# Optimization experiments

Measured on AMD Instinct MI355X. Metric: run time of the kernel, lower is better.

## Reference

```python
import jax, jax.numpy as jnp
import numpy as np

BETA = 0.25  # commitment loss weight (init kwarg)


def setup_inputs() -> dict:
    key = jax.random.key(0)
    k1, k2 = jax.random.split(key)
    z = jax.random.normal(k1, (16, 256, 32, 32), dtype=jnp.float32)
    embedding = jax.random.normal(k2, (8192, 256), dtype=jnp.float32)
    return {"z": z, "embedding": embedding}


def reference(z, embedding):
    # z: [B, C, H, W]  embedding: [K, C]
    B, C, H, W = z.shape
    zp = jnp.transpose(z, (0, 2, 3, 1))            # [B, H, W, C]
    zf = zp.reshape(-1, C)                          # [N, C]
    # squared euclidean distances via ||z||^2 + ||e||^2 - 2 z.e : [N, K]
    d = (jnp.sum(zf * zf, axis=1, keepdims=True)
         + jnp.sum(embedding * embedding, axis=1)
         - 2.0 * jnp.einsum('nd,kd->nk', zf, embedding))
    min_encoding_indices = jnp.argmin(d, axis=1)    # [N]
    z_q = embedding[min_encoding_indices].reshape(zp.shape)  # [B, H, W, C]
    loss = (BETA * jnp.mean((jax.lax.stop_gradient(z_q) - zp) ** 2)
            + jnp.mean((z_q - jax.lax.stop_gradient(zp)) ** 2))
    # straight-through estimator
    z_q = zp + jax.lax.stop_gradient(z_q - zp)
    z_q = jnp.transpose(z_q, (0, 3, 1, 2))          # back to [B, C, H, W]
    return z_q, loss, min_encoding_indices
```

## Files before the change

### kernel.cpp

```cpp
#include <hip/hip_runtime.h>

typedef unsigned int u32;
typedef unsigned long long u64;

#define C_DIM 256
#define HW 1024
#define N_TOT 16384
#define K_DIM 8192
#define ZQ_SIZE 4194304
#define LOSS_OFF ZQ_SIZE
#define IDX_OFF (ZQ_SIZE + 1)

#define KRANGE 2048
#define MARGIN 2.0f
#define CAP 524288u
#define LCAP 8192u

#define WS_ENORM 0
#define WS_CNT 8192
#define WS_PACKED 16384
#define WS_FIDX 49152
#define WS_LPART 65536
#define WS_LIST 131072
#define WS_ZT32 1179648
#define WS_ZTB16 5373952
#define WS_EB16 7471104

typedef __attribute__((ext_vector_type(4))) float f32x4;
typedef __attribute__((ext_vector_type(8))) __bf16 bf16x8;
typedef __attribute__((ext_vector_type(8))) unsigned short u16x8;

__device__ __forceinline__ void gld_lds16(const void* g, void* l) {
    __builtin_amdgcn_global_load_lds(
        (const __attribute__((address_space(1))) u32*)g,
        (__attribute__((address_space(3))) u32*)l, 16, 0, 0);
}

__device__ __forceinline__ unsigned short f2bf(float f) {
    u32 u = __float_as_uint(f);
    u32 r = (u + 0x7FFFu + ((u >> 16) & 1u)) >> 16;
    return (unsigned short)r;
}

__global__ __launch_bounds__(256) void k_prep_e(const float* __restrict__ e,
                                                unsigned short* __restrict__ eb,
                                                float* __restrict__ enorm1) {
    int w = threadIdx.x >> 6, l = threadIdx.x & 63;
    int row = blockIdx.x * 4 + w;
    const float4 v = *reinterpret_cast<const float4*>(e + (size_t)row * C_DIM + l * 4);
    float s = v.x * v.x + v.y * v.y + v.z * v.z + v.w * v.w;
    #pragma unroll
    for (int off = 32; off; off >>= 1) s += __shfl_xor(s, off, 64);
    if (l == 0) enorm1[row] = s + 1024.0f;
    ushort4 h;
    h.x = f2bf(v.x); h.y = f2bf(v.y); h.z = f2bf(v.z); h.w = f2bf(v.w);
    *reinterpret_cast<ushort4*>(eb + (size_t)row * C_DIM + l * 4) = h;
}

__global__ __launch_bounds__(256) void k_prep_z(const float* __restrict__ z,
                                                float* __restrict__ zt32,
                                                unsigned short* __restrict__ ztb) {
    int bid = blockIdx.x;
    int b = bid >> 7;
    int hwt = (bid >> 3) & 15;
    int ct = bid & 7;
    int t = threadIdx.x;
    __shared__ float tile[32][65];
    #pragma unroll
    for (int p = 0; p < 8; ++p) {
        int cl = p * 4 + (t >> 6), hl = t & 63;
        tile[cl][hl] = z[((size_t)b << 18) + ((size_t)(ct * 32 + cl) << 10) + hwt * 64 + hl];
    }
    __syncthreads();
    int hl = t & 63, cg = t >> 6;
    int n = (b << 10) + hwt * 64 + hl;
    float v[8];
    #pragma unroll
    for (int j = 0; j < 8; ++j) v[j] = tile[cg * 8 + j][hl];
    size_t base = (size_t)n * C_DIM + ct * 32 + cg * 8;
    *reinterpret_cast<float4*>(zt32 + base) = make_float4(v[0], v[1], v[2], v[3]);
    *reinterpret_cast<float4*>(zt32 + base + 4) = make_float4(v[4], v[5], v[6], v[7]);
    u16x8 h;
    #pragma unroll
    for (int j = 0; j < 8; ++j) h[j] = f2bf(v[j]);
    *reinterpret_cast<u16x8*>(ztb + base) = h;
}

__global__ __launch_bounds__(256, 2) void k_screen(const unsigned short* __restrict__ zt,
                                                   const unsigned short* __restrict__ et,
                                                   const float* __restrict__ enorm1,
                                                   u32* __restrict__ cnt,
                                                   uint2* __restrict__ list) {
    __shared__ __align__(16) char lds[81920];
    char* Ab = lds;
    char* Bb = lds + 65536;

    int logical = (blockIdx.x & 7) * 64 + (blockIdx.x >> 3);
    const int ks = logical >> 7;
    const int rowtile = logical & 127;
    const int n0 = rowtile * 128;
    const int kbase = ks * KRANGE;

    const int tid = threadIdx.x;
    const int l = tid & 63, w = tid >> 6;
    const int wr = w >> 1, wc = w & 1;
    const int ll = l & 15, lh = l >> 4;

    #pragma unroll
    for (int j = 0; j < 16; ++j) {
        int Y = (w * 16 + j) * 1024 + l * 16;
        int row = Y >> 9;
        int slot = (Y >> 4) & 31;
        const char* src = (const char*)zt + (((size_t)(n0 + row)) << 9) + ((slot ^ (row & 7)) << 4);
        gld_lds16(src, Ab + (w * 16 + j) * 1024);
    }

    const char* srcB[2];
    char* dstB[2];
    #pragma unroll
    for (int j = 0; j < 2; ++j) {
        int D = w * 128 + j * 64 + l;
        int rB = D >> 2;
        int sB = (D & 3) ^ ((rB >> 1) & 3);
        srcB[j] = (const char*)et + ((size_t)(kbase + rB) << 9) + (sB << 4);
        dstB[j] = Bb + (w * 128 + j * 64) * 16;
    }

    int aoff[4], rxA[4];
    #pragma unroll
    for (int mf = 0; mf < 4; ++mf) {
        int row = wr * 64 + mf * 16 + ll;
        aoff[mf] = row * 512;
        rxA[mf] = row & 7;
    }
    int bfrOff[4];
    #pragma unroll
    for (int kf = 0; kf < 4; ++kf) {
        int row = wc * 64 + kf * 16 + ll;
        bfrOff[kf] = (row * 4 + (lh ^ ((row >> 1) & 3))) * 16;
    }

    f32x4 acc[4][4];
    #pragma unroll
    for (int a = 0; a < 4; ++a)
        #pragma unroll
        for (int b = 0; b < 4; ++b) acc[a][b] = (f32x4){0.f, 0.f, 0.f, 0.f};
    float m1[16], m2[16];
    #pragma unroll
    for (int s = 0; s < 16; ++s) { m1[s] = 3.4e38f; m2[s] = 3.4e38f; }

    gld_lds16(srcB[0], dstB[0]);
    gld_lds16(srcB[1], dstB[1]);
    __syncthreads();

    for (int it = 0; it < 16; ++it) {
        float en[4];
        #pragma unroll
        for (int kf = 0; kf < 4; ++kf)
            en[kf] = enorm1[kbase + it * 128 + wc * 64 + kf * 16 + ll];

        #pragma unroll
        for (int cs = 0; cs < 8; ++cs) {
            const int p = cs & 1;
            if (it < 15 || cs < 7) {
                const size_t koff = (size_t)it * 65536 + ((cs == 7) ? 65536 : (cs + 1) * 64);
                gld_lds16(srcB[0] + koff, dstB[0] + (p ^ 1) * 8192);
                gld_lds16(srcB[1] + koff, dstB[1] + (p ^ 1) * 8192);
            }
            bf16x8 af[4], bfr[4];
            #pragma unroll
            for (int mf = 0; mf < 4; ++mf)
                af[mf] = *reinterpret_cast<const bf16x8*>(
                    Ab + aoff[mf] + (((cs * 4 + lh) ^ rxA[mf]) << 4));
            #pragma unroll
            for (int kf = 0; kf < 4; ++kf)
                bfr[kf] = *reinterpret_cast<const bf16x8*>(Bb + p * 8192 + bfrOff[kf]);
            __builtin_amdgcn_s_setprio(1);
            #pragma unroll
            for (int mf = 0; mf < 4; ++mf)
                #pragma unroll
                for (int kf = 0; kf < 4; ++kf)
                    acc[mf][kf] = __builtin_amdgcn_mfma_f32_16x16x32_bf16(
                        af[mf], bfr[kf], acc[mf][kf], 0, 0, 0);
            __builtin_amdgcn_s_setprio(0);

            if (cs == 7) {
                #pragma unroll
                for (int kf = 0; kf < 4; ++kf) {
                    const u32 kcol = (u32)(kbase + it * 128 + wc * 64 + kf * 16 + ll);
                    #pragma unroll
                    for (int mf = 0; mf < 4; ++mf) {
                        #pragma unroll
                        for (int r = 0; r < 4; ++r) {
                            float d = fmaf(-2.0f, acc[mf][kf][r], en[kf]);
                            float df = __uint_as_float((__float_as_uint(d) & 0xFFFFE000u) | kcol);
                            const int s2 = mf * 4 + r;
                            float t = fmaxf(m1[s2], df);
                            m2[s2] = fminf(m2[s2], t);
                            m1[s2] = fminf(m1[s2], df);
                            acc[mf][kf][r] = 0.0f;
                        }
                    }
                }
            }
            __syncthreads();
        }
    }

    float rowm[16];
    #pragma unroll
    for (int s = 0; s < 16; ++s) rowm[s] = m1[s];
    #pragma unroll
    for (int m = 1; m <= 8; m <<= 1)
        #pragma unroll
        for (int s = 0; s < 16; ++s)
            rowm[s] = fminf(rowm[s], __shfl_xor(rowm[s], m, 64));

    float* LDSrm = (float*)Bb;
    float* LDSrmF = (float*)(Bb + 1024);
    u32* ccnt = (u32*)(Bb + 1536);
    u32* gbase = (u32*)(Bb + 1540);
    uint2* cbuf = (uint2*)Ab;

    if (ll == 0) {
        #pragma unroll
        for (int s = 0; s < 16; ++s) {
            int row_local = wr * 64 + (s >> 2) * 16 + lh * 4 + (s & 3);
            LDSrm[row_local * 2 + wc] = rowm[s];
        }
    }
    if (tid == 0) *ccnt = 0;
    __syncthreads();
    if (tid < 128)
        LDSrmF[tid] = fminf(LDSrm[tid * 2], LDSrm[tid * 2 + 1]);
    __syncthreads();

    #pragma unroll
    for (int s = 0; s < 16; ++s) {
        int row_local = wr * 64 + (s >> 2) * 16 + lh * 4 + (s & 3);
        float rm = __uint_as_float(__float_as_uint(LDSrmF[row_local]) & 0xFFFFE000u);
        float d1 = __uint_as_float(__float_as_uint(m1[s]) & 0xFFFFE000u);
        if (d1 <= rm + MARGIN) {
            u32 pos = atomicAdd(ccnt, 1u);
            uint2 ent = make_uint2((u32)(n0 + row_local), __float_as_uint(m1[s]) & 8191u);
            if (pos < LCAP) cbuf[pos] = ent;
            else { u32 gp = atomicAdd(cnt, 1u); if (gp < CAP) list[gp] = ent; }
        }
        float d2 = __uint_as_float(__float_as_uint(m2[s]) & 0xFFFFE000u);
        if (d2 <= rm + MARGIN) {
            for (int it2 = 0; it2 < 16; ++it2) {
                #pragma unroll
                for (int kf = 0; kf < 4; ++kf) {
                    u32 k = (u32)(kbase + it2 * 128 + wc * 64 + kf * 16 + ll);
                    u32 pos = atomicAdd(ccnt, 1u);
                    uint2 ent = make_uint2((u32)(n0 + row_local), k);
                    if (pos < LCAP) cbuf[pos] = ent;
                    else { u32 gp = atomicAdd(cnt, 1u); if (gp < CAP) list[gp] = ent; }
                }
            }
        }
    }
    __syncthreads();
    if (tid == 0) {
        u32 total = *ccnt; if (total > LCAP) total = LCAP;
        *gbase = atomicAdd(cnt, total);
    }
    __syncthreads();
    u32 total = *ccnt; if (total > LCAP) total = LCAP;
    u32 gb = *gbase;
    for (u32 i = tid; i < total; i += 256) {
        u32 gp = gb + i;
        if (gp < CAP) list[gp] = cbuf[i];
    }
}

__global__ __launch_bounds__(256) void k_exact(const float* __restrict__ zt32,
                                               const float* __restrict__ e,
                                               const float* __restrict__ enorm1,
                                               const u32* __restrict__ cnt,
                                               const uint2* __restrict__ list,
                                               u64* __restrict__ packed) {
    const int nw = gridDim.x * 4;
    const int wid = blockIdx.x * 4 + (threadIdx.x >> 6);
    const int l = threadIdx.x & 63;
    u32 total = *cnt;
    if (total > CAP) total = CAP;
    for (u32 i = wid; i < total; i += nw) {
        uint2 c = list[i];
        const float4 zv = *reinterpret_cast<const float4*>(zt32 + (size_t)c.x * C_DIM + l * 4);
        const float4 ev = *reinterpret_cast<const float4*>(e + (size_t)c.y * C_DIM + l * 4);
        float s = zv.x * ev.x + zv.y * ev.y + zv.z * ev.z + zv.w * ev.w;
        #pragma unroll
        for (int off = 32; off; off >>= 1) s += __shfl_xor(s, off, 64);
        if (l == 0) {
            float d = fmaf(-2.0f, s, enorm1[c.y]);
            u32 ub = __float_as_uint(d);
            ub = (ub & 0x80000000u) ? ~ub : (ub | 0x80000000u);
            u64 key = ((u64)ub << 32) | (u64)c.y;
            atomicMin(packed + c.x, key);
        }
    }
}

__global__ __launch_bounds__(256) void k_fin(const u64* __restrict__ packed,
                                             int* __restrict__ fidx,
                                             float* __restrict__ out_idx) {
    int n = blockIdx.x * 256 + threadIdx.x;
    if (n >= N_TOT) return;
    u32 kk = (u32)(packed[n] & 0xFFFFFFFFull);
    if (kk > 8191u) kk = 0u;
    fidx[n] = (int)kk;
    out_idx[n] = (float)kk;
}

#define GBLOCKS 2048
__global__ __launch_bounds__(256) void k_gather(const float* __restrict__ z,
                                                const float* __restrict__ e,
                                                const int* __restrict__ fidx,
                                                float* __restrict__ zq,
                                                float* __restrict__ lpart) {
    float s = 0.0f;
    for (int i = blockIdx.x * 256 + threadIdx.x; i < ZQ_SIZE; i += GBLOCKS * 256) {
        int bb = i >> 18;
        int c = (i >> 10) & 255;
        int hw = i & 1023;
        int n = (bb << 10) | hw;
        float q = e[(size_t)fidx[n] * C_DIM + c];
        float zv = z[i];
        zq[i] = q;
        float d = q - zv;
        s = fmaf(d, d, s);
    }
    #pragma unroll
    for (int off = 32; off; off >>= 1) s += __shfl_xor(s, off, 64);
    __shared__ float wsum[4];
    int lane = threadIdx.x & 63, w = threadIdx.x >> 6;
    if (lane == 0) wsum[w] = s;
    __syncthreads();
    if (threadIdx.x == 0) lpart[blockIdx.x] = wsum[0] + wsum[1] + wsum[2] + wsum[3];
}

__global__ __launch_bounds__(256) void k_loss(const float* __restrict__ lpart,
                                              float* __restrict__ out_loss) {
    float s = 0.0f;
    for (int i = threadIdx.x; i < GBLOCKS; i += 256) s += lpart[i];
    #pragma unroll
    for (int off = 32; off; off >>= 1) s += __shfl_xor(s, off, 64);
    __shared__ float wsum[4];
    int lane = threadIdx.x & 63, w = threadIdx.x >> 6;
    if (lane == 0) wsum[w] = s;
    __syncthreads();
    if (threadIdx.x == 0)
        out_loss[0] = (wsum[0] + wsum[1] + wsum[2] + wsum[3]) * (1.25f / (float)ZQ_SIZE);
}

extern "C" void kernel_launch(void* const* d_in, const int* in_sizes, int n_in,
                              void* d_out, int out_size, void* d_ws, size_t ws_size,
                              hipStream_t stream) {
    const float* z = (const float*)d_in[0];
    const float* e = (const float*)d_in[1];
    float* out = (float*)d_out;
    float* ws = (float*)d_ws;

    float* enorm1 = ws + WS_ENORM;
    u32* cnt = (u32*)(ws + WS_CNT);
    u64* packed = (u64*)(ws + WS_PACKED);
    int* fidx = (int*)(ws + WS_FIDX);
    float* lpart = ws + WS_LPART;
    uint2* list = (uint2*)(ws + WS_LIST);
    float* zt32 = ws + WS_ZT32;
    unsigned short* ztb = (unsigned short*)(ws + WS_ZTB16);
    unsigned short* eb = (unsigned short*)(ws + WS_EB16);

    hipMemsetAsync(cnt, 0, sizeof(u32), stream);
    hipMemsetAsync(packed, 0xFF, (size_t)N_TOT * sizeof(u64), stream);

    k_prep_e<<<dim3(K_DIM / 4), dim3(256), 0, stream>>>(e, eb, enorm1);
    k_prep_z<<<dim3(2048), dim3(256), 0, stream>>>(z, zt32, ztb);
    k_screen<<<dim3(512), dim3(256), 0, stream>>>(ztb, eb, enorm1, cnt, list);
    k_exact<<<dim3(1024), dim3(256), 0, stream>>>(zt32, e, enorm1, cnt, list, packed);
    k_fin<<<dim3(64), dim3(256), 0, stream>>>(packed, fidx, out + IDX_OFF);
    k_gather<<<dim3(GBLOCKS), dim3(256), 0, stream>>>(z, e, fidx, out, lpart);
    k_loss<<<dim3(1), dim3(256), 0, stream>>>(lpart, out + LOSS_OFF);
}
```

Baseline: 194.2 us.

## Load codebook fragments directly into registers in screen kernel; fuse finalize into gather

The screening GEMM no longer stages the bf16 codebook through double-buffered LDS. Each lane now loads its B fragments straight from global memory into registers, ping-ponging between two register sets, which removes the per-step __syncthreads and shrinks LDS use. The separate k_fin kernel is folded into k_gather, which decodes the packed argmin key itself and writes the index output. The trade is more scattered global and L2 traffic for B in place of LDS reuse across waves, plus one fewer launch.

```diff
diff --git a/kernel.cpp b/kernel.cpp
--- a/kernel.cpp
+++ b/kernel.cpp
@@ -19,7 +19,6 @@
 #define WS_ENORM 0
 #define WS_CNT 8192
 #define WS_PACKED 16384
-#define WS_FIDX 49152
 #define WS_LPART 65536
 #define WS_LIST 131072
 #define WS_ZT32 1179648
@@ -91,9 +90,8 @@
                                                    const float* __restrict__ enorm1,
                                                    u32* __restrict__ cnt,
                                                    uint2* __restrict__ list) {
-    __shared__ __align__(16) char lds[81920];
+    __shared__ __align__(16) char lds[67088];
     char* Ab = lds;
-    char* Bb = lds + 65536;
 
     int logical = (blockIdx.x & 7) * 64 + (blockIdx.x >> 3);
     const int ks = logical >> 7;
@@ -115,17 +113,6 @@
         gld_lds16(src, Ab + (w * 16 + j) * 1024);
     }
 
-    const char* srcB[2];
-    char* dstB[2];
-    #pragma unroll
-    for (int j = 0; j < 2; ++j) {
-        int D = w * 128 + j * 64 + l;
-        int rB = D >> 2;
-        int sB = (D & 3) ^ ((rB >> 1) & 3);
-        srcB[j] = (const char*)et + ((size_t)(kbase + rB) << 9) + (sB << 4);
-        dstB[j] = Bb + (w * 128 + j * 64) * 16;
-    }
-
     int aoff[4], rxA[4];
     #pragma unroll
     for (int mf = 0; mf < 4; ++mf) {
@@ -133,12 +120,8 @@
         aoff[mf] = row * 512;
         rxA[mf] = row & 7;
     }
-    int bfrOff[4];
-    #pragma unroll
-    for (int kf = 0; kf < 4; ++kf) {
-        int row = wc * 64 + kf * 16 + ll;
-        bfrOff[kf] = (row * 4 + (lh ^ ((row >> 1) & 3))) * 16;
-    }
+
+    const char* ebB = (const char*)et + (((size_t)(kbase + wc * 64 + ll)) << 9) + lh * 16;
 
     f32x4 acc[4][4];
     #pragma unroll
@@ -149,61 +132,78 @@
     #pragma unroll
     for (int s = 0; s < 16; ++s) { m1[s] = 3.4e38f; m2[s] = 3.4e38f; }
 
-    gld_lds16(srcB[0], dstB[0]);
-    gld_lds16(srcB[1], dstB[1]);
+    bf16x8 bE[4], bO[4];
+    #pragma unroll
+    for (int kf = 0; kf < 4; ++kf)
+        bE[kf] = *reinterpret_cast<const bf16x8*>(ebB + kf * 8192);
+
     __syncthreads();
 
     for (int it = 0; it < 16; ++it) {
+        const size_t itoff = (size_t)it << 16;
         float en[4];
         #pragma unroll
         for (int kf = 0; kf < 4; ++kf)
             en[kf] = enorm1[kbase + it * 128 + wc * 64 + kf * 16 + ll];
 
         #pragma unroll
-        for (int cs = 0; cs < 8; ++cs) {
-            const int p = cs & 1;
-            if (it < 15 || cs < 7) {
-                const size_t koff = (size_t)it * 65536 + ((cs == 7) ? 65536 : (cs + 1) * 64);
-                gld_lds16(srcB[0] + koff, dstB[0] + (p ^ 1) * 8192);
-                gld_lds16(srcB[1] + koff, dstB[1] + (p ^ 1) * 8192);
-            }
-            bf16x8 af[4], bfr[4];
-            #pragma unroll
-            for (int mf = 0; mf < 4; ++mf)
-                af[mf] = *reinterpret_cast<const bf16x8*>(
-                    Ab + aoff[mf] + (((cs * 4 + lh) ^ rxA[mf]) << 4));
+        for (int cs = 0; cs < 8; cs += 2) {
             #pragma unroll
             for (int kf = 0; kf < 4; ++kf)
-                bfr[kf] = *reinterpret_cast<const bf16x8*>(Bb + p * 8192 + bfrOff[kf]);
-            __builtin_amdgcn_s_setprio(1);
+                bO[kf] = *reinterpret_cast<const bf16x8*>(ebB + itoff + kf * 8192 + (cs + 1) * 64);
+            {
+                bf16x8 af[4];
+                #pragma unroll
+                for (int mf = 0; mf < 4; ++mf)
+                    af[mf] = *reinterpret_cast<const bf16x8*>(
+                        Ab + aoff[mf] + (((cs * 4 + lh) ^ rxA[mf]) << 4));
+                __builtin_amdgcn_s_setprio(1);
+                #pragma unroll
+                for (int mf = 0; mf < 4; ++mf)
+                    #pragma unroll
+                    for (int kf = 0; kf < 4; ++kf)
+                        acc[mf][kf] = __builtin_amdgcn_mfma_f32_16x16x32_bf16(
+                            af[mf], bE[kf], acc[mf][kf], 0, 0, 0);
+                __builtin_amdgcn_s_setprio(0);
+            }
+            {
+                const size_t noff = (cs == 6) ? ((it < 15) ? itoff + 65536 : 0)
+                                              : itoff + (cs + 2) * 64;
+                #pragma unroll
+                for (int kf = 0; kf < 4; ++kf)
+                    bE[kf] = *reinterpret_cast<const bf16x8*>(ebB + noff + kf * 8192);
+                bf16x8 af[4];
+                #pragma unroll
+                for (int mf = 0; mf < 4; ++mf)
+                    af[mf] = *reinterpret_cast<const bf16x8*>(
+                        Ab + aoff[mf] + ((((cs + 1) * 4 + lh) ^ rxA[mf]) << 4));
+                __builtin_amdgcn_s_setprio(1);
+                #pragma unroll
+                for (int mf = 0; mf < 4; ++mf)
+                    #pragma unroll
+                    for (int kf = 0; kf < 4; ++kf)
+                        acc[mf][kf] = __builtin_amdgcn_mfma_f32_16x16x32_bf16(
+                            af[mf], bO[kf], acc[mf][kf], 0, 0, 0);
+                __builtin_amdgcn_s_setprio(0);
+            }
+        }
+
+        #pragma unroll
+        for (int kf = 0; kf < 4; ++kf) {
+            const u32 kcol = (u32)(kbase + it * 128 + wc * 64 + kf * 16 + ll);
             #pragma unroll
-            for (int mf = 0; mf < 4; ++mf)
-                #pragma unroll
-                for (int kf = 0; kf < 4; ++kf)
-                    acc[mf][kf] = __builtin_amdgcn_mfma_f32_16x16x32_bf16(
-                        af[mf], bfr[kf], acc[mf][kf], 0, 0, 0);
-            __builtin_amdgcn_s_setprio(0);
-
-            if (cs == 7) {
-                #pragma unroll
-                for (int kf = 0; kf < 4; ++kf) {
-                    const u32 kcol = (u32)(kbase + it * 128 + wc * 64 + kf * 16 + ll);
-                    #pragma unroll
-                    for (int mf = 0; mf < 4; ++mf) {
-                        #pragma unroll
-                        for (int r = 0; r < 4; ++r) {
-                            float d = fmaf(-2.0f, acc[mf][kf][r], en[kf]);
-                            float df = __uint_as_float((__float_as_uint(d) & 0xFFFFE000u) | kcol);
-                            const int s2 = mf * 4 + r;
-                            float t = fmaxf(m1[s2], df);
-                            m2[s2] = fminf(m2[s2], t);
-                            m1[s2] = fminf(m1[s2], df);
-                            acc[mf][kf][r] = 0.0f;
-                        }
-                    }
+            for (int mf = 0; mf < 4; ++mf) {
+                #pragma unroll
+                for (int r = 0; r < 4; ++r) {
+                    float d = fmaf(-2.0f, acc[mf][kf][r], en[kf]);
+                    float df = __uint_as_float((__float_as_uint(d) & 0xFFFFE000u) | kcol);
+                    const int s2 = mf * 4 + r;
+                    float t = fmaxf(m1[s2], df);
+                    m2[s2] = fminf(m2[s2], t);
+                    m1[s2] = fminf(m1[s2], df);
+                    acc[mf][kf][r] = 0.0f;
                 }
             }
-            __syncthreads();
         }
     }
 
@@ -216,10 +216,10 @@
         for (int s = 0; s < 16; ++s)
             rowm[s] = fminf(rowm[s], __shfl_xor(rowm[s], m, 64));
 
-    float* LDSrm = (float*)Bb;
-    float* LDSrmF = (float*)(Bb + 1024);
-    u32* ccnt = (u32*)(Bb + 1536);
-    u32* gbase = (u32*)(Bb + 1540);
+    float* LDSrm = (float*)(lds + 65536);
+    float* LDSrmF = (float*)(lds + 66560);
+    u32* ccnt = (u32*)(lds + 67072);
+    u32* gbase = (u32*)(lds + 67076);
     uint2* cbuf = (uint2*)Ab;
 
     if (ll == 0) {
@@ -302,32 +302,25 @@
     }
 }
 
-__global__ __launch_bounds__(256) void k_fin(const u64* __restrict__ packed,
-                                             int* __restrict__ fidx,
-                                             float* __restrict__ out_idx) {
-    int n = blockIdx.x * 256 + threadIdx.x;
-    if (n >= N_TOT) return;
-    u32 kk = (u32)(packed[n] & 0xFFFFFFFFull);
-    if (kk > 8191u) kk = 0u;
-    fidx[n] = (int)kk;
-    out_idx[n] = (float)kk;
-}
-
 #define GBLOCKS 2048
 __global__ __launch_bounds__(256) void k_gather(const float* __restrict__ z,
                                                 const float* __restrict__ e,
-                                                const int* __restrict__ fidx,
+                                                const u64* __restrict__ packed,
                                                 float* __restrict__ zq,
-                                                float* __restrict__ lpart) {
+                                                float* __restrict__ lpart,
+                                                float* __restrict__ out_idx) {
     float s = 0.0f;
     for (int i = blockIdx.x * 256 + threadIdx.x; i < ZQ_SIZE; i += GBLOCKS * 256) {
         int bb = i >> 18;
         int c = (i >> 10) & 255;
         int hw = i & 1023;
         int n = (bb << 10) | hw;
-        float q = e[(size_t)fidx[n] * C_DIM + c];
+        u32 kk = (u32)(packed[n] & 0xFFFFFFFFull);
+        if (kk > 8191u) kk = 0u;
+        float q = e[(size_t)kk * C_DIM + c];
         float zv = z[i];
         zq[i] = q;
+        if (c == 0) out_idx[n] = (float)kk;
         float d = q - zv;
         s = fmaf(d, d, s);
     }
@@ -365,7 +358,6 @@
     float* enorm1 = ws + WS_ENORM;
     u32* cnt = (u32*)(ws + WS_CNT);
     u64* packed = (u64*)(ws + WS_PACKED);
-    int* fidx = (int*)(ws + WS_FIDX);
     float* lpart = ws + WS_LPART;
     uint2* list = (uint2*)(ws + WS_LIST);
     float* zt32 = ws + WS_ZT32;
@@ -379,7 +371,6 @@
     k_prep_z<<<dim3(2048), dim3(256), 0, stream>>>(z, zt32, ztb);
     k_screen<<<dim3(512), dim3(256), 0, stream>>>(ztb, eb, enorm1, cnt, list);
     k_exact<<<dim3(1024), dim3(256), 0, stream>>>(zt32, e, enorm1, cnt, list, packed);
-    k_fin<<<dim3(64), dim3(256), 0, stream>>>(packed, fidx, out + IDX_OFF);
-    k_gather<<<dim3(GBLOCKS), dim3(256), 0, stream>>>(z, e, fidx, out, lpart);
+    k_gather<<<dim3(GBLOCKS), dim3(256), 0, stream>>>(z, e, packed, out, lpart, out + IDX_OFF);
     k_loss<<<dim3(1), dim3(256), 0, stream>>>(lpart, out + LOSS_OFF);
 }
```

After: 245.8 us. 1.27x slower.

## Widen screen GEMM to 512 threads with triple-buffered B loads and LDS norms

Applied to the files above, without the earlier changes.

The bf16 screening GEMM now uses 512-thread blocks (8 waves, 2x4 layout), so each block covers 256 codebook columns per iteration instead of 128. B tiles are triple-buffered and prefetched two stages ahead, using explicit vmcnt waits and raw barriers in place of full __syncthreads. The embedding norms are staged into LDS once rather than re-read from global memory each iteration. The aim is better MFMA utilisation and less load latency and sync stall, at the cost of higher LDS use (about 123 KB) and one block per CU.

```diff
diff --git a/kernel.cpp b/kernel.cpp
--- a/kernel.cpp
+++ b/kernel.cpp
@@ -86,14 +86,15 @@
     *reinterpret_cast<u16x8*>(ztb + base) = h;
 }
 
-__global__ __launch_bounds__(256, 2) void k_screen(const unsigned short* __restrict__ zt,
+__global__ __launch_bounds__(512, 1) void k_screen(const unsigned short* __restrict__ zt,
                                                    const unsigned short* __restrict__ et,
                                                    const float* __restrict__ enorm1,
                                                    u32* __restrict__ cnt,
                                                    uint2* __restrict__ list) {
-    __shared__ __align__(16) char lds[81920];
+    __shared__ __align__(16) char lds[125952];
     char* Ab = lds;
     char* Bb = lds + 65536;
+    float* eldsF = (float*)(lds + 114688);
 
     int logical = (blockIdx.x & 7) * 64 + (blockIdx.x >> 3);
     const int ks = logical >> 7;
@@ -103,28 +104,29 @@
 
     const int tid = threadIdx.x;
     const int l = tid & 63, w = tid >> 6;
-    const int wr = w >> 1, wc = w & 1;
+    const int wr = w >> 2, wc = w & 3;
     const int ll = l & 15, lh = l >> 4;
 
     #pragma unroll
-    for (int j = 0; j < 16; ++j) {
-        int Y = (w * 16 + j) * 1024 + l * 16;
+    for (int j = 0; j < 8; ++j) {
+        int Y = (w * 8 + j) * 1024 + l * 16;
         int row = Y >> 9;
         int slot = (Y >> 4) & 31;
         const char* src = (const char*)zt + (((size_t)(n0 + row)) << 9) + ((slot ^ (row & 7)) << 4);
-        gld_lds16(src, Ab + (w * 16 + j) * 1024);
-    }
-
-    const char* srcB[2];
-    char* dstB[2];
+        gld_lds16(src, Ab + (w * 8 + j) * 1024);
+    }
+    {
+        const char* src = (const char*)(enorm1 + kbase) + w * 1024 + l * 16;
+        gld_lds16(src, lds + 114688 + w * 1024);
+    }
+    const char* bsrcJ[2];
     #pragma unroll
     for (int j = 0; j < 2; ++j) {
-        int D = w * 128 + j * 64 + l;
-        int rB = D >> 2;
-        int sB = (D & 3) ^ ((rB >> 1) & 3);
-        srcB[j] = (const char*)et + ((size_t)(kbase + rB) << 9) + (sB << 4);
-        dstB[j] = Bb + (w * 128 + j * 64) * 16;
-    }
+        int D = (j * 8 + w) * 64 + l;
+        int rB = D >> 2, cB = D & 3;
+        bsrcJ[j] = (const char*)et + ((size_t)(kbase + rB) << 9) + ((cB ^ ((rB >> 1) & 3)) << 4);
+    }
+    const int bdst0 = (0 * 8 + w) * 1024, bdst1 = (1 * 8 + w) * 1024;
 
     int aoff[4], rxA[4];
     #pragma unroll
@@ -137,7 +139,7 @@
     #pragma unroll
     for (int kf = 0; kf < 4; ++kf) {
         int row = wc * 64 + kf * 16 + ll;
-        bfrOff[kf] = (row * 4 + (lh ^ ((row >> 1) & 3))) * 16;
+        bfrOff[kf] = row * 64 + ((lh ^ ((row >> 1) & 3)) << 4);
     }
 
     f32x4 acc[4][4];
@@ -149,24 +151,29 @@
     #pragma unroll
     for (int s = 0; s < 16; ++s) { m1[s] = 3.4e38f; m2[s] = 3.4e38f; }
 
-    gld_lds16(srcB[0], dstB[0]);
-    gld_lds16(srcB[1], dstB[1]);
-    __syncthreads();
-
-    for (int it = 0; it < 16; ++it) {
-        float en[4];
-        #pragma unroll
-        for (int kf = 0; kf < 4; ++kf)
-            en[kf] = enorm1[kbase + it * 128 + wc * 64 + kf * 16 + ll];
-
+    gld_lds16(bsrcJ[0], Bb + bdst0);
+    gld_lds16(bsrcJ[1], Bb + bdst1);
+    gld_lds16(bsrcJ[0] + 64, Bb + 16384 + bdst0);
+    gld_lds16(bsrcJ[1] + 64, Bb + 16384 + bdst1);
+    asm volatile("s_waitcnt vmcnt(2)" ::: "memory");
+    __builtin_amdgcn_s_barrier();
+    __builtin_amdgcn_sched_barrier(0);
+
+    int bsel = 0;
+    for (int it = 0; it < 8; ++it) {
         #pragma unroll
         for (int cs = 0; cs < 8; ++cs) {
-            const int p = cs & 1;
-            if (it < 15 || cs < 7) {
-                const size_t koff = (size_t)it * 65536 + ((cs == 7) ? 65536 : (cs + 1) * 64);
-                gld_lds16(srcB[0] + koff, dstB[0] + (p ^ 1) * 8192);
-                gld_lds16(srcB[1] + koff, dstB[1] + (p ^ 1) * 8192);
+            const int cs2 = (cs + 2) & 7;
+            const int itadd = (cs + 2) >> 3;
+            bool do_stage = (cs < 6) || (it < 7);
+            if (do_stage) {
+                int ssel = bsel + 2; if (ssel >= 3) ssel -= 3;
+                const size_t soff = (size_t)(it + itadd) * 131072 + (size_t)(cs2 * 64);
+                gld_lds16(bsrcJ[0] + soff, Bb + ssel * 16384 + bdst0);
+                gld_lds16(bsrcJ[1] + soff, Bb + ssel * 16384 + bdst1);
             }
+            __builtin_amdgcn_sched_barrier(0);
+            const char* bufp = Bb + bsel * 16384;
             bf16x8 af[4], bfr[4];
             #pragma unroll
             for (int mf = 0; mf < 4; ++mf)
@@ -174,7 +181,7 @@
                     Ab + aoff[mf] + (((cs * 4 + lh) ^ rxA[mf]) << 4));
             #pragma unroll
             for (int kf = 0; kf < 4; ++kf)
-                bfr[kf] = *reinterpret_cast<const bf16x8*>(Bb + p * 8192 + bfrOff[kf]);
+                bfr[kf] = *reinterpret_cast<const bf16x8*>(bufp + bfrOff[kf]);
             __builtin_amdgcn_s_setprio(1);
             #pragma unroll
             for (int mf = 0; mf < 4; ++mf)
@@ -187,12 +194,13 @@
             if (cs == 7) {
                 #pragma unroll
                 for (int kf = 0; kf < 4; ++kf) {
-                    const u32 kcol = (u32)(kbase + it * 128 + wc * 64 + kf * 16 + ll);
+                    float en = eldsF[it * 256 + wc * 64 + kf * 16 + ll];
+                    const u32 kcol = (u32)(kbase + it * 256 + wc * 64 + kf * 16 + ll);
                     #pragma unroll
                     for (int mf = 0; mf < 4; ++mf) {
                         #pragma unroll
                         for (int r = 0; r < 4; ++r) {
-                            float d = fmaf(-2.0f, acc[mf][kf][r], en[kf]);
+                            float d = fmaf(-2.0f, acc[mf][kf][r], en);
                             float df = __uint_as_float((__float_as_uint(d) & 0xFFFFE000u) | kcol);
                             const int s2 = mf * 4 + r;
                             float t = fmaxf(m1[s2], df);
@@ -203,7 +211,17 @@
                     }
                 }
             }
-            __syncthreads();
+            if (!(it == 7 && cs == 7)) {
+                if (cs == 6) {
+                    if (it == 7) { asm volatile("s_waitcnt vmcnt(0)" ::: "memory"); }
+                    else         { asm volatile("s_waitcnt vmcnt(2)" ::: "memory"); }
+                } else {
+                    asm volatile("s_waitcnt vmcnt(2)" ::: "memory");
+                }
+                __builtin_amdgcn_s_barrier();
+                __builtin_amdgcn_sched_barrier(0);
+            }
+            bsel = bsel + 1; if (bsel >= 3) bsel -= 3;
         }
     }
 
@@ -216,23 +234,24 @@
         for (int s = 0; s < 16; ++s)
             rowm[s] = fminf(rowm[s], __shfl_xor(rowm[s], m, 64));
 
-    float* LDSrm = (float*)Bb;
-    float* LDSrmF = (float*)(Bb + 1024);
-    u32* ccnt = (u32*)(Bb + 1536);
-    u32* gbase = (u32*)(Bb + 1540);
+    float* LDSrm = (float*)(lds + 122880);
+    float* LDSrmF = (float*)(lds + 124928);
+    u32* ccnt = (u32*)(lds + 125440);
+    u32* gbase = (u32*)(lds + 125444);
     uint2* cbuf = (uint2*)Ab;
 
     if (ll == 0) {
         #pragma unroll
         for (int s = 0; s < 16; ++s) {
             int row_local = wr * 64 + (s >> 2) * 16 + lh * 4 + (s & 3);
-            LDSrm[row_local * 2 + wc] = rowm[s];
+            LDSrm[row_local * 4 + wc] = rowm[s];
         }
     }
     if (tid == 0) *ccnt = 0;
     __syncthreads();
     if (tid < 128)
-        LDSrmF[tid] = fminf(LDSrm[tid * 2], LDSrm[tid * 2 + 1]);
+        LDSrmF[tid] = fminf(fminf(LDSrm[tid * 4], LDSrm[tid * 4 + 1]),
+                            fminf(LDSrm[tid * 4 + 2], LDSrm[tid * 4 + 3]));
     __syncthreads();
 
     #pragma unroll
@@ -248,10 +267,10 @@
         }
         float d2 = __uint_as_float(__float_as_uint(m2[s]) & 0xFFFFE000u);
         if (d2 <= rm + MARGIN) {
-            for (int it2 = 0; it2 < 16; ++it2) {
+            for (int it2 = 0; it2 < 8; ++it2) {
                 #pragma unroll
                 for (int kf = 0; kf < 4; ++kf) {
-                    u32 k = (u32)(kbase + it2 * 128 + wc * 64 + kf * 16 + ll);
+                    u32 k = (u32)(kbase + it2 * 256 + wc * 64 + kf * 16 + ll);
                     u32 pos = atomicAdd(ccnt, 1u);
                     uint2 ent = make_uint2((u32)(n0 + row_local), k);
                     if (pos < LCAP) cbuf[pos] = ent;
@@ -268,7 +287,7 @@
     __syncthreads();
     u32 total = *ccnt; if (total > LCAP) total = LCAP;
     u32 gb = *gbase;
-    for (u32 i = tid; i < total; i += 256) {
+    for (u32 i = tid; i < total; i += 512) {
         u32 gp = gb + i;
         if (gp < CAP) list[gp] = cbuf[i];
     }
@@ -377,7 +396,7 @@
 
     k_prep_e<<<dim3(K_DIM / 4), dim3(256), 0, stream>>>(e, eb, enorm1);
     k_prep_z<<<dim3(2048), dim3(256), 0, stream>>>(z, zt32, ztb);
-    k_screen<<<dim3(512), dim3(256), 0, stream>>>(ztb, eb, enorm1, cnt, list);
+    k_screen<<<dim3(512), dim3(512), 0, stream>>>(ztb, eb, enorm1, cnt, list);
     k_exact<<<dim3(1024), dim3(256), 0, stream>>>(zt32, e, enorm1, cnt, list, packed);
     k_fin<<<dim3(64), dim3(256), 0, stream>>>(packed, fidx, out + IDX_OFF);
     k_gather<<<dim3(GBLOCKS), dim3(256), 0, stream>>>(z, e, fidx, out, lpart);
```

After: 217.6 us. 1.12x slower.

## Keep z tile A-fragments in registers instead of LDS in screen kernel

Applied to the files above, without the earlier changes.

The screen kernel now loads each wave's 64x256 bf16 A-fragments directly from global memory into 32 VGPR vectors once, rather than staging the whole 128-row z tile in LDS and rereading it every k-step. This removes the per-step LDS reads for A and cuts shared memory from 80KB to about 66KB. The cost is 128 extra VGPRs per thread, which under launch_bounds(256,2) raises register pressure and risks spilling. The LDS scratch layout used by the epilogue is remapped to match.

```diff
diff --git a/kernel.cpp b/kernel.cpp
--- a/kernel.cpp
+++ b/kernel.cpp
@@ -36,6 +36,12 @@
         (__attribute__((address_space(3))) u32*)l, 16, 0, 0);
 }
 
+__device__ __forceinline__ bf16x8 gload16(const void* p) {
+    bf16x8 r;
+    asm volatile("global_load_dwordx4 %0, %1, off" : "=v"(r) : "v"(p));
+    return r;
+}
+
 __device__ __forceinline__ unsigned short f2bf(float f) {
     u32 u = __float_as_uint(f);
     u32 r = (u + 0x7FFFu + ((u >> 16) & 1u)) >> 16;
@@ -91,9 +97,8 @@
                                                    const float* __restrict__ enorm1,
                                                    u32* __restrict__ cnt,
                                                    uint2* __restrict__ list) {
-    __shared__ __align__(16) char lds[81920];
-    char* Ab = lds;
-    char* Bb = lds + 65536;
+    __shared__ __align__(16) char lds[67088];
+    char* Bb = lds;
 
     int logical = (blockIdx.x & 7) * 64 + (blockIdx.x >> 3);
     const int ks = logical >> 7;
@@ -105,15 +110,6 @@
     const int l = tid & 63, w = tid >> 6;
     const int wr = w >> 1, wc = w & 1;
     const int ll = l & 15, lh = l >> 4;
-
-    #pragma unroll
-    for (int j = 0; j < 16; ++j) {
-        int Y = (w * 16 + j) * 1024 + l * 16;
-        int row = Y >> 9;
-        int slot = (Y >> 4) & 31;
-        const char* src = (const char*)zt + (((size_t)(n0 + row)) << 9) + ((slot ^ (row & 7)) << 4);
-        gld_lds16(src, Ab + (w * 16 + j) * 1024);
-    }
 
     const char* srcB[2];
     char* dstB[2];
@@ -125,14 +121,6 @@
         srcB[j] = (const char*)et + ((size_t)(kbase + rB) << 9) + (sB << 4);
         dstB[j] = Bb + (w * 128 + j * 64) * 16;
     }
-
-    int aoff[4], rxA[4];
-    #pragma unroll
-    for (int mf = 0; mf < 4; ++mf) {
-        int row = wr * 64 + mf * 16 + ll;
-        aoff[mf] = row * 512;
-        rxA[mf] = row & 7;
-    }
     int bfrOff[4];
     #pragma unroll
     for (int kf = 0; kf < 4; ++kf) {
@@ -140,6 +128,19 @@
         bfrOff[kf] = (row * 4 + (lh ^ ((row >> 1) & 3))) * 16;
     }
 
+    gld_lds16(srcB[0], dstB[0]);
+    gld_lds16(srcB[1], dstB[1]);
+
+    const char* abase = (const char*)zt + (((size_t)(n0 + wr * 64 + ll)) << 9) + lh * 16;
+    bf16x8 afr[4][8];
+    #pragma unroll
+    for (int mf = 0; mf < 4; ++mf)
+        #pragma unroll
+        for (int q = 0; q < 8; ++q)
+            afr[mf][q] = gload16(abase + mf * 8192 + q * 64);
+    asm volatile("s_waitcnt vmcnt(0)" ::: "memory");
+    __builtin_amdgcn_sched_barrier(0);
+
     f32x4 acc[4][4];
     #pragma unroll
     for (int a = 0; a < 4; ++a)
@@ -149,8 +150,6 @@
     #pragma unroll
     for (int s = 0; s < 16; ++s) { m1[s] = 3.4e38f; m2[s] = 3.4e38f; }
 
-    gld_lds16(srcB[0], dstB[0]);
-    gld_lds16(srcB[1], dstB[1]);
     __syncthreads();
 
     for (int it = 0; it < 16; ++it) {
@@ -167,11 +166,7 @@
                 gld_lds16(srcB[0] + koff, dstB[0] + (p ^ 1) * 8192);
                 gld_lds16(srcB[1] + koff, dstB[1] + (p ^ 1) * 8192);
             }
-            bf16x8 af[4], bfr[4];
-            #pragma unroll
-            for (int mf = 0; mf < 4; ++mf)
-                af[mf] = *reinterpret_cast<const bf16x8*>(
-                    Ab + aoff[mf] + (((cs * 4 + lh) ^ rxA[mf]) << 4));
+            bf16x8 bfr[4];
             #pragma unroll
             for (int kf = 0; kf < 4; ++kf)
                 bfr[kf] = *reinterpret_cast<const bf16x8*>(Bb + p * 8192 + bfrOff[kf]);
@@ -181,7 +176,7 @@
                 #pragma unroll
                 for (int kf = 0; kf < 4; ++kf)
                     acc[mf][kf] = __builtin_amdgcn_mfma_f32_16x16x32_bf16(
-                        af[mf], bfr[kf], acc[mf][kf], 0, 0, 0);
+                        afr[mf][cs], bfr[kf], acc[mf][kf], 0, 0, 0);
             __builtin_amdgcn_s_setprio(0);
 
             if (cs == 7) {
@@ -216,11 +211,11 @@
         for (int s = 0; s < 16; ++s)
             rowm[s] = fminf(rowm[s], __shfl_xor(rowm[s], m, 64));
 
-    float* LDSrm = (float*)Bb;
-    float* LDSrmF = (float*)(Bb + 1024);
-    u32* ccnt = (u32*)(Bb + 1536);
-    u32* gbase = (u32*)(Bb + 1540);
-    uint2* cbuf = (uint2*)Ab;
+    float* LDSrm = (float*)(lds + 65536);
+    float* LDSrmF = (float*)(lds + 66560);
+    u32* ccnt = (u32*)(lds + 67072);
+    u32* gbase = (u32*)(lds + 67076);
+    uint2* cbuf = (uint2*)lds;
 
     if (ll == 0) {
         #pragma unroll
```

Result: slower. 227.9 us (+17.4%).
